# Kernel tuning notes

Hardware: AMD Instinct MI355X
Metric: run time of the kernel (lower is better)

Reference implementation:

```python
import jax, jax.numpy as jnp
import numpy as np

N_MI, N_DI = 100000, 50000   # node counts
E, L = 500000, 200000        # message edges, supervision (label) edges
F_MI, F_DI, H = 256, 128, 128


def setup_inputs() -> dict:
    key = jax.random.key(0)
    ks = iter(jax.random.split(key, 40))

    def nrm(shape, scale):
        return jax.random.normal(next(ks), shape, jnp.float32) * scale

    inp = {
        'x_mi': jax.random.normal(next(ks), (N_MI, F_MI), jnp.float32),
        'x_di': jax.random.normal(next(ks), (N_DI, F_DI), jnp.float32),
        'W_mi': nrm((H, F_MI), 1.0 / np.sqrt(F_MI)),
        'b_mi': jnp.zeros((H,), jnp.float32),
        'W_di': nrm((H, F_DI), 1.0 / np.sqrt(F_DI)),
        'b_di': jnp.zeros((H,), jnp.float32),
        'emb_mi': nrm((N_MI, H), 1.0),
        'emb_di': nrm((N_DI, H), 1.0),
    }
    # SAGEConv weights per layer per relation (md: miRNA->disease, dm: reverse)
    dims = [(H, 256), (256, 128), (128, 64)]
    for i, (ci, co) in enumerate(dims, 1):
        for rel in ('md', 'dm'):
            inp[f'Wl{i}_{rel}'] = nrm((co, ci), 1.0 / np.sqrt(ci))  # neighbor lin (with bias)
            inp[f'bl{i}_{rel}'] = jnp.zeros((co,), jnp.float32)
            inp[f'Wr{i}_{rel}'] = nrm((co, ci), 1.0 / np.sqrt(ci))  # root lin (no bias)
    inp['edge_src'] = jax.random.randint(next(ks), (E,), 0, N_MI)
    inp['edge_dst'] = jax.random.randint(next(ks), (E,), 0, N_DI)
    inp['label_src'] = jax.random.randint(next(ks), (L,), 0, N_MI)
    inp['label_dst'] = jax.random.randint(next(ks), (L,), 0, N_DI)
    return inp


def _sage(x_src, x_dst, src, dst, n_dst, Wl, bl, Wr):
    # PyG SAGEConv (mean aggr): out = lin_l(mean_neighbors) + lin_r(x_dst)
    agg = jax.ops.segment_sum(x_src[src], dst, num_segments=n_dst)
    deg = jax.ops.segment_sum(jnp.ones_like(dst, dtype=x_src.dtype), dst, num_segments=n_dst)
    mean = agg / jnp.maximum(deg, 1.0)[:, None]
    return mean @ Wl.T + bl + x_dst @ Wr.T


def reference(x_mi, x_di, W_mi, b_mi, W_di, b_di, emb_mi, emb_di,
              Wl1_md, bl1_md, Wr1_md, Wl1_dm, bl1_dm, Wr1_dm,
              Wl2_md, bl2_md, Wr2_md, Wl2_dm, bl2_dm, Wr2_dm,
              Wl3_md, bl3_md, Wr3_md, Wl3_dm, bl3_dm, Wr3_dm,
              edge_src, edge_dst, label_src, label_dst):
    # node_id == arange(num_nodes), so the embedding lookup is the full table
    h_mi = x_mi @ W_mi.T + b_mi + emb_mi
    h_di = x_di @ W_di.T + b_di + emb_di
    layers = [((Wl1_md, bl1_md, Wr1_md), (Wl1_dm, bl1_dm, Wr1_dm)),
              ((Wl2_md, bl2_md, Wr2_md), (Wl2_dm, bl2_dm, Wr2_dm)),
              ((Wl3_md, bl3_md, Wr3_md), (Wl3_dm, bl3_dm, Wr3_dm))]
    for li, (pmd, pdm) in enumerate(layers):
        new_di = _sage(h_mi, h_di, edge_src, edge_dst, N_DI, *pmd)  # miRNA -> disease
        new_mi = _sage(h_di, h_mi, edge_dst, edge_src, N_MI, *pdm)  # disease -> miRNA (reverse)
        if li < 2:
            new_mi, new_di = jax.nn.relu(new_mi), jax.nn.relu(new_di)
        h_mi, h_di = new_mi, new_di
    # classifier: dot product on supervision edges -> [L]
    return (h_mi[label_src] * h_di[label_dst]).sum(axis=-1)
```

## Files before the change

### kernel.cpp

```cpp
#include <hip/hip_runtime.h>

#define N_MI 100000
#define N_DI 50000
#define MI_P 100352
#define DI_P 50176

#define SCAN_CHUNK 2048
#define NB_DI ((N_DI + SCAN_CHUNK - 1) / SCAN_CHUNK)
#define NB_MI ((N_MI + SCAN_CHUNK - 1) / SCAN_CHUNK)

typedef _Float16 half8  __attribute__((ext_vector_type(8)));
typedef _Float16 half4  __attribute__((ext_vector_type(4)));
typedef float    floatx4 __attribute__((ext_vector_type(4)));

__global__ __launch_bounds__(256) void scan_part_kernel(const int* __restrict__ deg_di,
                                                        const int* __restrict__ deg_mi,
                                                        int* __restrict__ row_di,
                                                        int* __restrict__ row_mi,
                                                        int* __restrict__ bsum) {
    const int* deg; int* row; int n; int* bs;
    if (blockIdx.y == 0) { deg = deg_di; row = row_di; n = N_DI; bs = bsum; }
    else                 { deg = deg_mi; row = row_mi; n = N_MI; bs = bsum + 64; }
    int nb = (n + SCAN_CHUNK - 1) / SCAN_CHUNK;
    if ((int)blockIdx.x >= nb) return;
    int t = threadIdx.x;
    int base = blockIdx.x * SCAN_CHUNK + t * 8;
    int v[8]; int s = 0;
    #pragma unroll
    for (int e = 0; e < 8; ++e) {
        int i = base + e;
        v[e] = (i < n) ? deg[i] : 0;
        s += v[e];
    }
    int lane = t & 63, w = t >> 6;
    int x = s;
    #pragma unroll
    for (int off = 1; off < 64; off <<= 1) {
        int y = __shfl_up(x, off, 64);
        if (lane >= off) x += y;
    }
    __shared__ int wsum[4];
    if (lane == 63) wsum[w] = x;
    __syncthreads();
    int woff = 0;
    #pragma unroll
    for (int i = 0; i < 3; ++i) if (i < w) woff += wsum[i];
    int run = woff + x - s;
    #pragma unroll
    for (int e = 0; e < 8; ++e) {
        int i = base + e;
        if (i < n) row[i] = run;
        run += v[e];
    }
    if (t == 255) bs[blockIdx.x] = woff + x;
}

__global__ void scan_sums_kernel(int* __restrict__ bsum, int* __restrict__ row_di,
                                 int* __restrict__ row_mi) {
    int w = threadIdx.x >> 6, lane = threadIdx.x & 63;
    int nb = (w == 0) ? NB_DI : NB_MI;
    int* bs = bsum + w * 64;
    int v = (lane < nb) ? bs[lane] : 0;
    int x = v;
    #pragma unroll
    for (int off = 1; off < 64; off <<= 1) {
        int y = __shfl_up(x, off, 64);
        if (lane >= off) x += y;
    }
    if (lane < nb) bs[lane] = x - v;
    if (lane == nb - 1) {
        if (w == 0) row_di[N_DI] = x;
        else        row_mi[N_MI] = x;
    }
}

__global__ __launch_bounds__(256) void scan_add_kernel(const int* __restrict__ bsum,
                                                       int* __restrict__ row_di,
                                                       int* __restrict__ row_mi) {
    int* row; int n; const int* bs;
    if (blockIdx.y == 0) { row = row_di; n = N_DI; bs = bsum; }
    else                 { row = row_mi; n = N_MI; bs = bsum + 64; }
    int nb = (n + SCAN_CHUNK - 1) / SCAN_CHUNK;
    int b = blockIdx.x;
    if (b >= nb || b == 0) return;
    int off = bs[b];
    int base = b * SCAN_CHUNK + threadIdx.x;
    #pragma unroll
    for (int e = 0; e < 8; ++e) {
        int i = base + e * 256;
        if (i < n) row[i] += off;
    }
}


struct CvtW {
    const float* s[14];
    _Float16* d[14];
    int K[14];
    int KI[14];
    int nch[14];
};

__device__ __forceinline__ void cvtw_body(const CvtW& a, int b) {
    int arr = b / 16;
    int c = (b % 16) * 256 + threadIdx.x;
    if (c >= a.nch[arr]) return;
    int K = a.K[arr], KI = a.KI[arr];
    int lane = c & 63;
    int j = (c >> 6) & 3;
    int rest = c >> 8;
    int k = rest % KI;
    int p = rest / KI;
    int row = p * 64 + j * 16 + (lane & 15);
    int kcol = k * 32 + (lane >> 4) * 8;
    const float* s = a.s[arr] + (long)row * K + kcol;
    float4 u = *(const float4*)s;
    float4 v = *(const float4*)(s + 4);
    half8 h = {(_Float16)u.x, (_Float16)u.y, (_Float16)u.z, (_Float16)u.w,
               (_Float16)v.x, (_Float16)v.y, (_Float16)v.z, (_Float16)v.w};
    *(half8*)(a.d[arr] + (long)c * 8) = h;
}

template<int K>
__device__ __forceinline__ void cvt_frag_body(const float* __restrict__ in,
                                              _Float16* __restrict__ out, int M,
                                              int tile, _Float16* lds) {
    constexpr int KI = K / 32;
    constexpr int CPR = K / 8;
    const int tid = threadIdx.x;
    #pragma unroll
    for (int it = 0; it < KI; ++it) {
        int c = tid + it * 256;
        int r = c / CPR, col = c % CPR;
        int row = tile * 64 + r;
        if (row >= M) row = M - 1;
        const float* g = in + (long)row * K + col * 8;
        float4 u = *(const float4*)g;
        float4 v = *(const float4*)(g + 4);
        half8 h = {(_Float16)u.x, (_Float16)u.y, (_Float16)u.z, (_Float16)u.w,
                   (_Float16)v.x, (_Float16)v.y, (_Float16)v.z, (_Float16)v.w};
        *(half8*)&lds[r * (K + 8) + col * 8] = h;
    }
    __syncthreads();
    #pragma unroll
    for (int it = 0; it < KI; ++it) {
        int c = tid + it * 256;
        int lane = c & 63, i = (c >> 6) & 3, k = c >> 8;
        half8 h = *(const half8*)&lds[(i * 16 + (lane & 15)) * (K + 8) + k * 32 + (lane >> 4) * 8];
        *(half8*)(out + ((long)tile * 8 * K + c) * 8) = h;
    }
}

struct Prep {
    const int* src; const int* dst;
    int* deg_mi; int* deg_di;
    int E; int ncount;
    CvtW cw;
    const float* xmi; const float* xdi;
    _Float16* ofmi; _Float16* ofdi;
};

__global__ __launch_bounds__(256) void prep_kernel(Prep a) {
    __shared__ _Float16 lds[64 * 264];
    int b = blockIdx.x;
    if (b < a.ncount) {
        int i = b * 256 + threadIdx.x;
        if (i < a.E) {
            atomicAdd(&a.deg_mi[a.src[i]], 1);
            atomicAdd(&a.deg_di[a.dst[i]], 1);
        }
        return;
    }
    b -= a.ncount;
    if (b < 224) { cvtw_body(a.cw, b); return; }
    b -= 224;
    if (b < MI_P / 64) { cvt_frag_body<256>(a.xmi, a.ofmi, N_MI, b, lds); return; }
    b -= MI_P / 64;
    cvt_frag_body<128>(a.xdi, a.ofdi, N_DI, b, lds);
}

template<int DIN>
__device__ __forceinline__ void agg2_body(const _Float16* __restrict__ hsrc,
                                          const int* __restrict__ row,
                                          const int* __restrict__ csr,
                                          _Float16* __restrict__ outf, int n, int blk) {
    constexpr int LPR = DIN / 8;
    constexpr int GR  = 64 / LPR;
    constexpr int KI  = DIN / 32;
    int node = blk * 4 + (threadIdx.x >> 6);
    if (node >= n) return;
    int lane = threadIdx.x & 63;
    int g = lane / LPR, c = lane % LPR;
    int beg = row[node], end = row[node + 1];
    float acc[8] = {};
    #pragma unroll 2
    for (int j = beg + g; j < end; j += GR) {
        half8 v = *(const half8*)(hsrc + (long)csr[j] * DIN + c * 8);
        #pragma unroll
        for (int e = 0; e < 8; ++e) acc[e] += (float)v[e];
    }
    float inv = 1.f / (float)max(end - beg, 1);
    half8 o;
    #pragma unroll
    for (int e = 0; e < 8; ++e) {
        float s = acc[e];
        s += __shfl_down(s, 32);
        if (GR == 4) s += __shfl_down(s, 16);
        o[e] = (_Float16)(s * inv);
    }
    if (g == 0) {
        int mt = node >> 6, ii = (node >> 4) & 3, lrm = node & 15;
        long off = (((long)mt * KI + (c >> 2)) * 4 + ii) * 512 + (lrm + 16 * (c & 3)) * 8;
        *(half8*)(outf + off) = o;
    }
}

struct FusedAgg {
    const _Float16* hmi; const _Float16* hdi;
    const int* row_di; const int* csr_di;
    const int* row_mi; const int* csr_mi;
    _Float16* outdi; _Float16* outmi;
    int nmib;
};

template<int DIN>
__global__ __launch_bounds__(256) void fused_agg_kernel(FusedAgg a) {
    int b = blockIdx.x;
    if (b < a.nmib) agg2_body<DIN>(a.hdi, a.row_mi, a.csr_mi, a.outmi, N_MI, b);
    else            agg2_body<DIN>(a.hmi, a.row_di, a.csr_di, a.outdi, N_DI, b - a.nmib);
}

template<int KI, bool DUAL, int MR, bool CADD>
__device__ __forceinline__ void hgemm_body(
    const _Float16* __restrict__ A1f, const _Float16* __restrict__ W1f,
    const _Float16* __restrict__ A2f, const _Float16* __restrict__ W2f,
    const float* __restrict__ bias, const float* __restrict__ Cadd,
    _Float16* __restrict__ C, _Float16* __restrict__ Cf,
    int M, int N, int relu, int bx, int p, _Float16* lds)
{
    const int wave = threadIdx.x >> 6, lane = threadIdx.x & 63;
    const int quad = lane >> 4, lr = lane & 15;
    const int g0 = (bx * 4 + wave) * MR;
    const int mt = g0 >> 2, i0 = g0 & 3;
    const long abase = ((long)(mt * KI * 4 + i0)) * 512 + lane * 8;
    const long wbase = ((long)p * KI * 4) * 512 + lane * 8;
    _Float16* lw = lds + wave * (MR * 16 * 72);

    floatx4 acc[MR][4] = {};

    #pragma unroll
    for (int pass = 0; pass < (DUAL ? 2 : 1); ++pass) {
        const _Float16* A = pass ? A2f : A1f;
        const _Float16* W = pass ? W2f : W1f;
        #pragma unroll
        for (int k = 0; k < KI; ++k) {
            half8 af[MR], bf[4];
            #pragma unroll
            for (int i = 0; i < MR; ++i)
                af[i] = *(const half8*)(A + abase + (k * 4 + i) * 512);
            #pragma unroll
            for (int j = 0; j < 4; ++j)
                bf[j] = *(const half8*)(W + wbase + (k * 4 + j) * 512);
            #pragma unroll
            for (int i = 0; i < MR; ++i)
                #pragma unroll
                for (int j = 0; j < 4; ++j)
                    acc[i][j] = __builtin_amdgcn_mfma_f32_16x16x32_f16(af[i], bf[j], acc[i][j], 0, 0, 0);
        }
    }

    const int m0 = g0 * 16, n0 = p * 64;
    #pragma unroll
    for (int ii = 0; ii < MR; ++ii) {
        #pragma unroll
        for (int j = 0; j < 4; ++j) {
            float bn = bias[n0 + j * 16 + lr];
            #pragma unroll
            for (int r = 0; r < 4; ++r) {
                float v = acc[ii][j][r] + bn;
                if (!CADD && relu) v = fmaxf(v, 0.f);
                lw[(ii * 16 + quad * 4 + r) * 72 + j * 16 + lr] = (_Float16)v;
            }
        }
    }
    __syncthreads();

    const int r2 = lane >> 3, cs = lane & 7;
    #pragma unroll
    for (int ii = 0; ii < MR * 2; ++ii) {
        int m = m0 + ii * 8 + r2;
        half8 h = *(const half8*)&lw[(ii * 8 + r2) * 72 + cs * 8];
        if (CADD) {
            if (m < M) {
                const float* g = Cadd + (long)m * N + n0 + cs * 8;
                float4 u = *(const float4*)g;
                float4 v = *(const float4*)(g + 4);
                float t[8] = {u.x, u.y, u.z, u.w, v.x, v.y, v.z, v.w};
                #pragma unroll
                for (int e = 0; e < 8; ++e) {
                    float x = (float)h[e] + t[e];
                    if (relu) x = fmaxf(x, 0.f);
                    h[e] = (_Float16)x;
                }
            }
            *(half8*)&lw[(ii * 8 + r2) * 72 + cs * 8] = h;
        }
        if (m < M)
            *(half8*)(C + (long)m * N + n0 + cs * 8) = h;
    }
    if (CADD) __syncthreads();

    if (Cf) {
        const int KIn = N >> 5;
        #pragma unroll
        for (int ii = 0; ii < MR; ++ii) {
            #pragma unroll
            for (int k2 = 0; k2 < 2; ++k2) {
                half8 h = *(const half8*)&lw[(ii * 16 + lr) * 72 + k2 * 32 + quad * 8];
                *(half8*)(Cf + ((long)(mt * KIn + p * 2 + k2) * 4 + i0 + ii) * 512 + lane * 8) = h;
            }
        }
    }
}

struct FusedGemm {
    const _Float16 *Ami, *Wlmi, *Rmi, *Wrmi; const float* bmi;
    _Float16 *Cmi, *Cfmi;
    const _Float16 *Adi, *Wldi, *Rdi, *Wrdi; const float* bdi;
    _Float16 *Cdi, *Cfdi;
    int nmib, xmi, xdi, Nmi, Ndi, relu;
};

template<int KI, int MRM, int MRD>
__global__ __launch_bounds__(256, 4) void fused_gemm_kernel(FusedGemm a) {
    constexpr int MRX = (MRM > MRD) ? MRM : MRD;
    __shared__ _Float16 lds[4 * MRX * 16 * 72];
    int b = blockIdx.x;
    if (b < a.nmib) {
        hgemm_body<KI, true, MRM, false>(a.Ami, a.Wlmi, a.Rmi, a.Wrmi, a.bmi, nullptr,
                                         a.Cmi, a.Cfmi, N_MI, a.Nmi, a.relu,
                                         b % a.xmi, b / a.xmi, lds);
    } else {
        b -= a.nmib;
        hgemm_body<KI, true, MRD, false>(a.Adi, a.Wldi, a.Rdi, a.Wrdi, a.bdi, nullptr,
                                         a.Cdi, a.Cfdi, N_DI, a.Ndi, a.relu,
                                         b % a.xdi, b / a.xdi, lds);
    }
}

struct FusedInit {
    const int* src; const int* dst;
    const int* row_mi; const int* row_di;
    int* cur_mi; int* cur_di; int* csr_mi; int* csr_di;
    int E; int nfill;
    const _Float16* Ami; const _Float16* Wmi; const float* bmi; const float* embmi;
    _Float16* Cmi; _Float16* Cfmi;
    const _Float16* Adi; const _Float16* Wdi; const float* bdi; const float* embdi;
    _Float16* Cdi; _Float16* Cfdi;
};

__global__ __launch_bounds__(256, 4) void fused_init_kernel(FusedInit a) {
    __shared__ _Float16 lds[4 * 2 * 16 * 72];
    int b = blockIdx.x;
    if (b < a.nfill) {
        int i = b * 256 + threadIdx.x;
        if (i < a.E) {
            int s = a.src[i], d = a.dst[i];
            int p = atomicAdd(&a.cur_di[d], 1);
            a.csr_di[a.row_di[d] + p] = s;
            int q = atomicAdd(&a.cur_mi[s], 1);
            a.csr_mi[a.row_mi[s] + q] = d;
        }
        return;
    }
    b -= a.nfill;
    if (b < (MI_P / 128) * 2) {
        hgemm_body<8, false, 2, true>(a.Ami, a.Wmi, nullptr, nullptr, a.bmi, a.embmi,
                                      a.Cmi, a.Cfmi, N_MI, 128, 0, b >> 1, b & 1, lds);
        return;
    }
    b -= (MI_P / 128) * 2;
    hgemm_body<4, false, 1, true>(a.Adi, a.Wdi, nullptr, nullptr, a.bdi, a.embdi,
                                  a.Cdi, a.Cfdi, N_DI, 128, 0, b >> 1, b & 1, lds);
}

__global__ void classify_kernel(const _Float16* __restrict__ hmi, const _Float16* __restrict__ hdi,
                                const int* __restrict__ ls, const int* __restrict__ ld,
                                float* __restrict__ out, int L) {
    long idx = (long)blockIdx.x * blockDim.x + threadIdx.x;
    int e = (int)(idx >> 4), q = (int)(idx & 15);
    if (e >= L) return;
    const half4* ra = (const half4*)(hmi + (long)ls[e] * 64);
    const half4* rb = (const half4*)(hdi + (long)ld[e] * 64);
    half4 a = ra[q], b = rb[q];
    float s = (float)a.x * (float)b.x + (float)a.y * (float)b.y +
              (float)a.z * (float)b.z + (float)a.w * (float)b.w;
    #pragma unroll
    for (int off = 8; off >= 1; off >>= 1) s += __shfl_down(s, off, 16);
    if (q == 0) out[e] = s;
}

extern "C" void kernel_launch(void* const* d_in, const int* in_sizes, int n_in,
                              void* d_out, int out_size, void* d_ws, size_t ws_size,
                              hipStream_t stream) {
    const float* x_mi   = (const float*)d_in[0];
    const float* x_di   = (const float*)d_in[1];
    const float* W_mi   = (const float*)d_in[2];
    const float* b_mi   = (const float*)d_in[3];
    const float* W_di   = (const float*)d_in[4];
    const float* b_di   = (const float*)d_in[5];
    const float* emb_mi = (const float*)d_in[6];
    const float* emb_di = (const float*)d_in[7];
    const float* Wl1_md = (const float*)d_in[8];
    const float* bl1_md = (const float*)d_in[9];
    const float* Wr1_md = (const float*)d_in[10];
    const float* Wl1_dm = (const float*)d_in[11];
    const float* bl1_dm = (const float*)d_in[12];
    const float* Wr1_dm = (const float*)d_in[13];
    const float* Wl2_md = (const float*)d_in[14];
    const float* bl2_md = (const float*)d_in[15];
    const float* Wr2_md = (const float*)d_in[16];
    const float* Wl2_dm = (const float*)d_in[17];
    const float* bl2_dm = (const float*)d_in[18];
    const float* Wr2_dm = (const float*)d_in[19];
    const float* Wl3_md = (const float*)d_in[20];
    const float* bl3_md = (const float*)d_in[21];
    const float* Wr3_md = (const float*)d_in[22];
    const float* Wl3_dm = (const float*)d_in[23];
    const float* bl3_dm = (const float*)d_in[24];
    const float* Wr3_dm = (const float*)d_in[25];
    const int* edge_src  = (const int*)d_in[26];
    const int* edge_dst  = (const int*)d_in[27];
    const int* label_src = (const int*)d_in[28];
    const int* label_dst = (const int*)d_in[29];
    const int E = in_sizes[26];
    const int L = in_sizes[28];
    float* out = (float*)d_out;

    _Float16* hp = (_Float16*)d_ws;
    _Float16* wWmi  = hp; hp += 128 * 256;
    _Float16* wWdi  = hp; hp += 128 * 128;
    _Float16* wl1md = hp; hp += 256 * 128;
    _Float16* wr1md = hp; hp += 256 * 128;
    _Float16* wl1dm = hp; hp += 256 * 128;
    _Float16* wr1dm = hp; hp += 256 * 128;
    _Float16* wl2md = hp; hp += 128 * 256;
    _Float16* wr2md = hp; hp += 128 * 256;
    _Float16* wl2dm = hp; hp += 128 * 256;
    _Float16* wr2dm = hp; hp += 128 * 256;
    _Float16* wl3md = hp; hp += 64 * 128;
    _Float16* wr3md = hp; hp += 64 * 128;
    _Float16* wl3dm = hp; hp += 64 * 128;
    _Float16* wr3dm = hp; hp += 64 * 128;
    _Float16* h_mi0 = hp; hp += (long)MI_P * 128;
    _Float16* h_mi1 = hp; hp += (long)MI_P * 256;
    _Float16* h_di0 = hp; hp += (long)DI_P * 128;
    _Float16* h_di1 = hp; hp += (long)DI_P * 256;
    _Float16* hfa_mi = hp; hp += (long)MI_P * 128;
    _Float16* hfb_mi = hp; hp += (long)MI_P * 256;
    _Float16* hfa_di = hp; hp += (long)DI_P * 128;
    _Float16* hfb_di = hp; hp += (long)DI_P * 256;
    _Float16* aggmi  = hp; hp += (long)MI_P * 256;
    _Float16* aggdi  = hp; hp += (long)DI_P * 256;

    int* ip = (int*)hp;
    int* deg_di = ip;  ip += N_DI;
    int* deg_mi = ip;  ip += N_MI;
    int* cur_di = ip;  ip += N_DI;
    int* cur_mi = ip;  ip += N_MI;
    int* row_di = ip;  ip += N_DI + 1;
    int* row_mi = ip;  ip += N_MI + 1;
    int* csr_di = ip;  ip += E;
    int* csr_mi = ip;  ip += E;
    int* bsum   = ip;  ip += 128;

    int eb = (E + 255) / 256;

    hipMemsetAsync(deg_di, 0, (size_t)(2 * (N_DI + N_MI)) * sizeof(int), stream);

    Prep pr;
    pr.src = edge_src; pr.dst = edge_dst;
    pr.deg_mi = deg_mi; pr.deg_di = deg_di;
    pr.E = E; pr.ncount = eb;
    const float* srcs[14] = {W_mi, W_di, Wl1_md, Wr1_md, Wl1_dm, Wr1_dm,
                             Wl2_md, Wr2_md, Wl2_dm, Wr2_dm, Wl3_md, Wr3_md, Wl3_dm, Wr3_dm};
    _Float16* dsts[14] = {wWmi, wWdi, wl1md, wr1md, wl1dm, wr1dm,
                          wl2md, wr2md, wl2dm, wr2dm, wl3md, wr3md, wl3dm, wr3dm};
    int Ks[14]  = {256, 128, 128, 128, 128, 128, 256, 256, 256, 256, 128, 128, 128, 128};
    int Ns[14]  = {128, 128, 256, 256, 256, 256, 128, 128, 128, 128, 64, 64, 64, 64};
    for (int i = 0; i < 14; ++i) {
        pr.cw.s[i] = srcs[i]; pr.cw.d[i] = dsts[i];
        pr.cw.K[i] = Ks[i]; pr.cw.KI[i] = Ks[i] / 32;
        pr.cw.nch[i] = Ns[i] * Ks[i] / 8;
    }
    pr.xmi = x_mi; pr.xdi = x_di; pr.ofmi = hfb_mi; pr.ofdi = hfb_di;
    int prep_blocks = eb + 224 + MI_P / 64 + DI_P / 64;
    prep_kernel<<<prep_blocks, 256, 0, stream>>>(pr);

    scan_part_kernel<<<dim3(NB_MI, 2), 256, 0, stream>>>(deg_di, deg_mi, row_di, row_mi, bsum);
    scan_sums_kernel<<<1, 128, 0, stream>>>(bsum, row_di, row_mi);
    scan_add_kernel<<<dim3(NB_MI, 2), 256, 0, stream>>>(bsum, row_di, row_mi);

    FusedInit fi;
    fi.src = edge_src; fi.dst = edge_dst;
    fi.row_mi = row_mi; fi.row_di = row_di;
    fi.cur_mi = cur_mi; fi.cur_di = cur_di;
    fi.csr_mi = csr_mi; fi.csr_di = csr_di;
    fi.E = E; fi.nfill = eb;
    fi.Ami = hfb_mi; fi.Wmi = wWmi; fi.bmi = b_mi; fi.embmi = emb_mi;
    fi.Cmi = h_mi0; fi.Cfmi = hfa_mi;
    fi.Adi = hfb_di; fi.Wdi = wWdi; fi.bdi = b_di; fi.embdi = emb_di;
    fi.Cdi = h_di0; fi.Cfdi = hfa_di;
    int fused_blocks = eb + (MI_P / 128) * 2 + (DI_P / 64) * 2;
    fused_init_kernel<<<fused_blocks, 256, 0, stream>>>(fi);

    const int nmib_agg = (N_MI + 3) / 4, ndib_agg = (N_DI + 3) / 4;

    {
        FusedAgg fa{h_mi0, h_di0, row_di, csr_di, row_mi, csr_mi, aggdi, aggmi, nmib_agg};
        fused_agg_kernel<128><<<nmib_agg + ndib_agg, 256, 0, stream>>>(fa);
        FusedGemm fg;
        fg.Ami = aggmi; fg.Wlmi = wl1dm; fg.Rmi = hfa_mi; fg.Wrmi = wr1dm; fg.bmi = bl1_dm;
        fg.Cmi = h_mi1; fg.Cfmi = hfb_mi;
        fg.Adi = aggdi; fg.Wldi = wl1md; fg.Rdi = hfa_di; fg.Wrdi = wr1md; fg.bdi = bl1_md;
        fg.Cdi = h_di1; fg.Cfdi = hfb_di;
        fg.xmi = MI_P / 128; fg.xdi = DI_P / 64;
        fg.nmib = fg.xmi * 4; fg.Nmi = 256; fg.Ndi = 256; fg.relu = 1;
        fused_gemm_kernel<4, 2, 1><<<fg.nmib + fg.xdi * 4, 256, 0, stream>>>(fg);
    }

    {
        FusedAgg fa{h_mi1, h_di1, row_di, csr_di, row_mi, csr_mi, aggdi, aggmi, nmib_agg};
        fused_agg_kernel<256><<<nmib_agg + ndib_agg, 256, 0, stream>>>(fa);
        FusedGemm fg;
        fg.Ami = aggmi; fg.Wlmi = wl2dm; fg.Rmi = hfb_mi; fg.Wrmi = wr2dm; fg.bmi = bl2_dm;
        fg.Cmi = h_mi0; fg.Cfmi = hfa_mi;
        fg.Adi = aggdi; fg.Wldi = wl2md; fg.Rdi = hfb_di; fg.Wrdi = wr2md; fg.bdi = bl2_md;
        fg.Cdi = h_di0; fg.Cfdi = hfa_di;
        fg.xmi = MI_P / 128; fg.xdi = DI_P / 64;
        fg.nmib = fg.xmi * 2; fg.Nmi = 128; fg.Ndi = 128; fg.relu = 1;
        fused_gemm_kernel<8, 2, 1><<<fg.nmib + fg.xdi * 2, 256, 0, stream>>>(fg);
    }

    {
        FusedAgg fa{h_mi0, h_di0, row_di, csr_di, row_mi, csr_mi, aggdi, aggmi, nmib_agg};
        fused_agg_kernel<128><<<nmib_agg + ndib_agg, 256, 0, stream>>>(fa);
        FusedGemm fg;
        fg.Ami = aggmi; fg.Wlmi = wl3dm; fg.Rmi = hfa_mi; fg.Wrmi = wr3dm; fg.bmi = bl3_dm;
        fg.Cmi = h_mi1; fg.Cfmi = nullptr;
        fg.Adi = aggdi; fg.Wldi = wl3md; fg.Rdi = hfa_di; fg.Wrdi = wr3md; fg.bdi = bl3_md;
        fg.Cdi = h_di1; fg.Cfdi = nullptr;
        fg.xmi = MI_P / 64; fg.xdi = DI_P / 64;
        fg.nmib = fg.xmi; fg.Nmi = 64; fg.Ndi = 64; fg.relu = 0;
        fused_gemm_kernel<4, 1, 1><<<fg.nmib + fg.xdi, 256, 0, stream>>>(fg);
    }

    classify_kernel<<<((long)L * 16 + 255) / 256, 256, 0, stream>>>(
        h_mi1, h_di1, label_src, label_dst, out, L);
}
```

Measured before the change: 767.0 us.

## Gather neighbor features from fragment layout, drop row-major activation copies

The aggregation kernel now reads neighbor rows directly from the MFMA fragment-layout buffers instead of separate row-major copies. The GEMM epilogues stop writing row-major outputs for the input projection and the first two layers, which removes redundant global stores of every intermediate activation. The cost is that each gathered 16-byte chunk now comes from a strided fragment address rather than a contiguous row, which can hurt gather coalescing and cache-line use.

```diff
diff --git a/kernel.cpp b/kernel.cpp
--- a/kernel.cpp
+++ b/kernel.cpp
@@ -180,7 +180,7 @@
 }
 
 template<int DIN>
-__device__ __forceinline__ void agg2_body(const _Float16* __restrict__ hsrc,
+__device__ __forceinline__ void agg2_body(const _Float16* __restrict__ hsrcf,
                                           const int* __restrict__ row,
                                           const int* __restrict__ csr,
                                           _Float16* __restrict__ outf, int n, int blk) {
@@ -191,11 +191,15 @@
     if (node >= n) return;
     int lane = threadIdx.x & 63;
     int g = lane / LPR, c = lane % LPR;
+    const int kc = c >> 2, cq = c & 3;
+    const long cbase = (long)kc * 4 * 512 + cq * 16 * 8;
     int beg = row[node], end = row[node + 1];
     float acc[8] = {};
     #pragma unroll 2
     for (int j = beg + g; j < end; j += GR) {
-        half8 v = *(const half8*)(hsrc + (long)csr[j] * DIN + c * 8);
+        int nd = csr[j];
+        long off = ((long)(nd >> 6) * KI * 4 + ((nd >> 4) & 3)) * 512 + (nd & 15) * 8 + cbase;
+        half8 v = *(const half8*)(hsrcf + off);
         #pragma unroll
         for (int e = 0; e < 8; ++e) acc[e] += (float)v[e];
     }
@@ -210,13 +214,13 @@
     }
     if (g == 0) {
         int mt = node >> 6, ii = (node >> 4) & 3, lrm = node & 15;
-        long off = (((long)mt * KI + (c >> 2)) * 4 + ii) * 512 + (lrm + 16 * (c & 3)) * 8;
+        long off = (((long)mt * KI + kc) * 4 + ii) * 512 + (lrm + 16 * cq) * 8;
         *(half8*)(outf + off) = o;
     }
 }
 
 struct FusedAgg {
-    const _Float16* hmi; const _Float16* hdi;
+    const _Float16* hmif; const _Float16* hdif;
     const int* row_di; const int* csr_di;
     const int* row_mi; const int* csr_mi;
     _Float16* outdi; _Float16* outmi;
@@ -226,8 +230,8 @@
 template<int DIN>
 __global__ __launch_bounds__(256) void fused_agg_kernel(FusedAgg a) {
     int b = blockIdx.x;
-    if (b < a.nmib) agg2_body<DIN>(a.hdi, a.row_mi, a.csr_mi, a.outmi, N_MI, b);
-    else            agg2_body<DIN>(a.hmi, a.row_di, a.csr_di, a.outdi, N_DI, b - a.nmib);
+    if (b < a.nmib) agg2_body<DIN>(a.hdif, a.row_mi, a.csr_mi, a.outmi, N_MI, b);
+    else            agg2_body<DIN>(a.hmif, a.row_di, a.csr_di, a.outdi, N_DI, b - a.nmib);
 }
 
 template<int KI, bool DUAL, int MR, bool CADD>
@@ -305,7 +309,7 @@
             }
             *(half8*)&lw[(ii * 8 + r2) * 72 + cs * 8] = h;
         }
-        if (m < M)
+        if (C && m < M)
             *(half8*)(C + (long)m * N + n0 + cs * 8) = h;
     }
     if (CADD) __syncthreads();
@@ -354,9 +358,9 @@
     int* cur_mi; int* cur_di; int* csr_mi; int* csr_di;
     int E; int nfill;
     const _Float16* Ami; const _Float16* Wmi; const float* bmi; const float* embmi;
-    _Float16* Cmi; _Float16* Cfmi;
+    _Float16* Cfmi;
     const _Float16* Adi; const _Float16* Wdi; const float* bdi; const float* embdi;
-    _Float16* Cdi; _Float16* Cfdi;
+    _Float16* Cfdi;
 };
 
 __global__ __launch_bounds__(256, 4) void fused_init_kernel(FusedInit a) {
@@ -376,12 +380,12 @@
     b -= a.nfill;
     if (b < (MI_P / 128) * 2) {
         hgemm_body<8, false, 2, true>(a.Ami, a.Wmi, nullptr, nullptr, a.bmi, a.embmi,
-                                      a.Cmi, a.Cfmi, N_MI, 128, 0, b >> 1, b & 1, lds);
+                                      nullptr, a.Cfmi, N_MI, 128, 0, b >> 1, b & 1, lds);
         return;
     }
     b -= (MI_P / 128) * 2;
     hgemm_body<4, false, 1, true>(a.Adi, a.Wdi, nullptr, nullptr, a.bdi, a.embdi,
-                                  a.Cdi, a.Cfdi, N_DI, 128, 0, b >> 1, b & 1, lds);
+                                  nullptr, a.Cfdi, N_DI, 128, 0, b >> 1, b & 1, lds);
 }
 
 __global__ void classify_kernel(const _Float16* __restrict__ hmi, const _Float16* __restrict__ hdi,
@@ -452,10 +456,8 @@
     _Float16* wr3md = hp; hp += 64 * 128;
     _Float16* wl3dm = hp; hp += 64 * 128;
     _Float16* wr3dm = hp; hp += 64 * 128;
-    _Float16* h_mi0 = hp; hp += (long)MI_P * 128;
-    _Float16* h_mi1 = hp; hp += (long)MI_P * 256;
-    _Float16* h_di0 = hp; hp += (long)DI_P * 128;
-    _Float16* h_di1 = hp; hp += (long)DI_P * 256;
+    _Float16* h_mi1 = hp; hp += (long)MI_P * 64;
+    _Float16* h_di1 = hp; hp += (long)DI_P * 64;
     _Float16* hfa_mi = hp; hp += (long)MI_P * 128;
     _Float16* hfb_mi = hp; hp += (long)MI_P * 256;
     _Float16* hfa_di = hp; hp += (long)DI_P * 128;
@@ -507,43 +509,41 @@
     fi.cur_mi = cur_mi; fi.cur_di = cur_di;
     fi.csr_mi = csr_mi; fi.csr_di = csr_di;
     fi.E = E; fi.nfill = eb;
-    fi.Ami = hfb_mi; fi.Wmi = wWmi; fi.bmi = b_mi; fi.embmi = emb_mi;
-    fi.Cmi = h_mi0; fi.Cfmi = hfa_mi;
-    fi.Adi = hfb_di; fi.Wdi = wWdi; fi.bdi = b_di; fi.embdi = emb_di;
-    fi.Cdi = h_di0; fi.Cfdi = hfa_di;
+    fi.Ami = hfb_mi; fi.Wmi = wWmi; fi.bmi = b_mi; fi.embmi = emb_mi; fi.Cfmi = hfa_mi;
+    fi.Adi = hfb_di; fi.Wdi = wWdi; fi.bdi = b_di; fi.embdi = emb_di; fi.Cfdi = hfa_di;
     int fused_blocks = eb + (MI_P / 128) * 2 + (DI_P / 64) * 2;
     fused_init_kernel<<<fused_blocks, 256, 0, stream>>>(fi);
 
     const int nmib_agg = (N_MI + 3) / 4, ndib_agg = (N_DI + 3) / 4;
 
     {
-        FusedAgg fa{h_mi0, h_di0, row_di, csr_di, row_mi, csr_mi, aggdi, aggmi, nmib_agg};
+        FusedAgg fa{hfa_mi, hfa_di, row_di, csr_di, row_mi, csr_mi, aggdi, aggmi, nmib_agg};
         fused_agg_kernel<128><<<nmib_agg + ndib_agg, 256, 0, stream>>>(fa);
         FusedGemm fg;
         fg.Ami = aggmi; fg.Wlmi = wl1dm; fg.Rmi = hfa_mi; fg.Wrmi = wr1dm; fg.bmi = bl1_dm;
-        fg.Cmi = h_mi1; fg.Cfmi = hfb_mi;
+        fg.Cmi = nullptr; fg.Cfmi = hfb_mi;
         fg.Adi = aggdi; fg.Wldi = wl1md; fg.Rdi = hfa_di; fg.Wrdi = wr1md; fg.bdi = bl1_md;
-        fg.Cdi = h_di1; fg.Cfdi = hfb_di;
+        fg.Cdi = nullptr; fg.Cfdi = hfb_di;
         fg.xmi = MI_P / 128; fg.xdi = DI_P / 64;
         fg.nmib = fg.xmi * 4; fg.Nmi = 256; fg.Ndi = 256; fg.relu = 1;
         fused_gemm_kernel<4, 2, 1><<<fg.nmib + fg.xdi * 4, 256, 0, stream>>>(fg);
     }
 
     {
-        FusedAgg fa{h_mi1, h_di1, row_di, csr_di, row_mi, csr_mi, aggdi, aggmi, nmib_agg};
+        FusedAgg fa{hfb_mi, hfb_di, row_di, csr_di, row_mi, csr_mi, aggdi, aggmi, nmib_agg};
         fused_agg_kernel<256><<<nmib_agg + ndib_agg, 256, 0, stream>>>(fa);
         FusedGemm fg;
         fg.Ami = aggmi; fg.Wlmi = wl2dm; fg.Rmi = hfb_mi; fg.Wrmi = wr2dm; fg.bmi = bl2_dm;
-        fg.Cmi = h_mi0; fg.Cfmi = hfa_mi;
+        fg.Cmi = nullptr; fg.Cfmi = hfa_mi;
         fg.Adi = aggdi; fg.Wldi = wl2md; fg.Rdi = hfb_di; fg.Wrdi = wr2md; fg.bdi = bl2_md;
-        fg.Cdi = h_di0; fg.Cfdi = hfa_di;
+        fg.Cdi = nullptr; fg.Cfdi = hfa_di;
         fg.xmi = MI_P / 128; fg.xdi = DI_P / 64;
         fg.nmib = fg.xmi * 2; fg.Nmi = 128; fg.Ndi = 128; fg.relu = 1;
         fused_gemm_kernel<8, 2, 1><<<fg.nmib + fg.xdi * 2, 256, 0, stream>>>(fg);
     }
 
     {
-        FusedAgg fa{h_mi0, h_di0, row_di, csr_di, row_mi, csr_mi, aggdi, aggmi, nmib_agg};
+        FusedAgg fa{hfa_mi, hfa_di, row_di, csr_di, row_mi, csr_mi, aggdi, aggmi, nmib_agg};
         fused_agg_kernel<128><<<nmib_agg + ndib_agg, 256, 0, stream>>>(fa);
         FusedGemm fg;
         fg.Ami = aggmi; fg.Wlmi = wl3dm; fg.Rmi = hfa_mi; fg.Wrmi = wr3dm; fg.bmi = bl3_dm;
```

Result: slower. 1.537 ms (+100.5%).
